# Kernel tuning notes

Measured on AMD Instinct MI355X. Metric: run time of the kernel, lower is better.

The kernel has to match this reference:

```python
import jax, jax.numpy as jnp
import numpy as np

N, E, D = 50000, 600000, 128
NEG_SLOPE = 0.2

def setup_inputs() -> dict:
    key = jax.random.key(0)
    ks = jax.random.split(key, 12)
    s = 1.0 / np.sqrt(D)
    return {
        "x": jax.random.normal(ks[0], (N, D), jnp.float32),
        "edge_index": jax.random.randint(ks[1], (2, E), 0, N),
        "edge_attr": jax.random.normal(ks[2], (E, D), jnp.float32),
        "ln1_g": jnp.ones((D,), jnp.float32),
        "ln1_b": jnp.zeros((D,), jnp.float32),
        "W_lin": jax.random.normal(ks[3], (D, D), jnp.float32) * s,
        "att_src": jax.random.normal(ks[4], (D,), jnp.float32) * s,
        "att_dst": jax.random.normal(ks[5], (D,), jnp.float32) * s,
        "W_edge": jax.random.normal(ks[6], (D, D), jnp.float32) * s,
        "att_edge": jax.random.normal(ks[7], (D,), jnp.float32) * s,
        "gat_bias": jnp.zeros((D,), jnp.float32),
        "ln2_g": jnp.ones((D,), jnp.float32),
        "ln2_b": jnp.zeros((D,), jnp.float32),
        "W1": jax.random.normal(ks[8], (D, 4 * D), jnp.float32) * s,
        "b1": jnp.zeros((4 * D,), jnp.float32),
        "W2": jax.random.normal(ks[9], (4 * D, D), jnp.float32) * (1.0 / np.sqrt(4 * D)),
        "b2": jnp.zeros((D,), jnp.float32),
    }


def _layernorm(x, g, b, eps=1e-5):
    mu = jnp.mean(x, axis=-1, keepdims=True)
    var = jnp.mean(jnp.square(x - mu), axis=-1, keepdims=True)
    return (x - mu) * jax.lax.rsqrt(var + eps) * g + b


def _gat_conv(x, edge_index, edge_attr, W_lin, att_src, att_dst, W_edge, att_edge, gat_bias):
    # PyG GATConv, heads=1, concat=False, add_self_loops=False, edge_dim=D
    src, dst = edge_index[0], edge_index[1]
    h = x @ W_lin                      # [N, D] shared src/dst projection
    a_src = h @ att_src                # [N]
    a_dst = h @ att_dst                # [N]
    a_edge = (edge_attr @ W_edge) @ att_edge  # [E]
    alpha = a_src[src] + a_dst[dst] + a_edge  # [E]
    alpha = jnp.where(alpha > 0, alpha, NEG_SLOPE * alpha)  # leaky_relu(0.2)
    # segment softmax over destination nodes
    m = jax.ops.segment_max(alpha, dst, num_segments=N)
    m = jnp.where(jnp.isfinite(m), m, 0.0)
    ex = jnp.exp(alpha - m[dst])
    denom = jax.ops.segment_sum(ex, dst, num_segments=N)
    coef = ex / jnp.maximum(denom[dst], 1e-16)
    # weighted scatter-aggregation of source messages
    out = jax.ops.segment_sum(coef[:, None] * h[src], dst, num_segments=N)
    return out + gat_bias


def reference(x, edge_index, edge_attr, ln1_g, ln1_b, W_lin, att_src, att_dst,
              W_edge, att_edge, gat_bias, ln2_g, ln2_b, W1, b1, W2, b2):
    # pre-norm + GAT message passing + residual (dropout = eval identity)
    xn = _layernorm(x, ln1_g, ln1_b)
    x = x + _gat_conv(xn, edge_index, edge_attr, W_lin, att_src, att_dst,
                      W_edge, att_edge, gat_bias)
    # pre-norm + FFN + residual
    xn = _layernorm(x, ln2_g, ln2_b)
    ffn = jax.nn.relu(xn @ W1 + b1) @ W2 + b2
    return x + ffn
```

## Files before the change

kernel.cpp:

```cpp
#include <hip/hip_runtime.h>

#define D 128
#define NEG_SLOPE 0.2f

typedef __attribute__((ext_vector_type(8))) short short8;
typedef __attribute__((ext_vector_type(4))) float f32x4;

__device__ __forceinline__ float wred_sum(float v){
#pragma unroll
  for (int m = 32; m; m >>= 1) v += __shfl_xor(v, m);
  return v;
}
__device__ __forceinline__ int wred_sumi(int v){
#pragma unroll
  for (int m = 32; m; m >>= 1) v += __shfl_xor(v, m);
  return v;
}
__device__ __forceinline__ float wred_max(float v){
#pragma unroll
  for (int m = 32; m; m >>= 1) v = fmaxf(v, __shfl_xor(v, m));
  return v;
}
__device__ __forceinline__ unsigned short bf16r(float f){
  unsigned int u = __float_as_uint(f);
  u += 0x7fffu + ((u >> 16) & 1u);
  return (unsigned short)(u >> 16);
}
__device__ __forceinline__ float bf2f(unsigned int hi16){
  return __uint_as_float(hi16 << 16);
}

__global__ void k_prep0(const float* __restrict__ W_lin, const float* __restrict__ W1,
                        const float* __restrict__ W2, const float* __restrict__ W_edge,
                        const float* __restrict__ att_edge,
                        unsigned short* __restrict__ Wlt, unsigned short* __restrict__ W1t,
                        unsigned short* __restrict__ W2t, float* __restrict__ we,
                        int* __restrict__ cnt, int N){
  int t = blockIdx.x * blockDim.x + threadIdx.x;
  if (t < N) cnt[t] = 0;
  if (t < 128 * 128){
    int c = t >> 7, k = t & 127;
    Wlt[t] = bf16r(W_lin[k * 128 + c]);
  } else if (t < 128 * 128 + 512 * 128){
    int u = t - 128 * 128; int c = u >> 7, k = u & 127;
    W1t[u] = bf16r(W1[k * 512 + c]);
  } else if (t < 128 * 128 + 512 * 128 + 128 * 512){
    int u = t - (128 * 128 + 512 * 128); int c = u >> 9, k = u & 511;
    W2t[u] = bf16r(W2[k * 128 + c]);
  } else {
    int u = t - (128 * 128 + 512 * 128 + 128 * 512);
    if (u < 128){
      float s = 0.f;
      for (int j = 0; j < 128; ++j) s += W_edge[u * 128 + j] * att_edge[j];
      we[u] = s;
    }
  }
}

__global__ __launch_bounds__(256) void k_hgemm(const float* __restrict__ x,
                                               const unsigned short* __restrict__ Wlt,
                                               const float* __restrict__ ln1_g,
                                               const float* __restrict__ ln1_b,
                                               const float* __restrict__ att_src,
                                               const float* __restrict__ att_dst,
                                               const int* __restrict__ ei,
                                               unsigned short* __restrict__ hq,
                                               float* __restrict__ asrc,
                                               float* __restrict__ adst,
                                               int* __restrict__ cnt, int N, int E){
  __shared__ unsigned short wbuf[16384];
#pragma unroll
  for (int r = 0; r < 8; ++r){
    int idx = r * 256 + threadIdx.x;
    int c = idx >> 4, kc = idx & 15;
    short8 w = *(const short8*)(Wlt + c * 128 + kc * 8);
    *(short8*)((char*)wbuf + c * 256 + ((kc * 16) ^ ((c & 7) << 4))) = w;
  }
  __syncthreads();
  int wid = threadIdx.x >> 6, lane = threadIdx.x & 63;
  int rb = blockIdx.x * 64 + wid * 16;
  int row = rb + (lane & 15);
  int rowc = row < N ? row : N - 1;
  int ksub = (lane >> 4) * 8;
  float v[4][8];
#pragma unroll
  for (int kb = 0; kb < 4; ++kb){
    float4 p0 = *(const float4*)(x + (size_t)rowc * 128 + kb * 32 + ksub);
    float4 p1 = *(const float4*)(x + (size_t)rowc * 128 + kb * 32 + ksub + 4);
    v[kb][0]=p0.x; v[kb][1]=p0.y; v[kb][2]=p0.z; v[kb][3]=p0.w;
    v[kb][4]=p1.x; v[kb][5]=p1.y; v[kb][6]=p1.z; v[kb][7]=p1.w;
  }
  float s = 0.f;
#pragma unroll
  for (int kb = 0; kb < 4; ++kb)
#pragma unroll
    for (int j = 0; j < 8; ++j) s += v[kb][j];
  s += __shfl_xor(s, 16); s += __shfl_xor(s, 32);
  float mu = s * (1.0f / 128.f);
  float q = 0.f;
#pragma unroll
  for (int kb = 0; kb < 4; ++kb)
#pragma unroll
    for (int j = 0; j < 8; ++j){ float d = v[kb][j] - mu; q += d * d; }
  q += __shfl_xor(q, 16); q += __shfl_xor(q, 32);
  float rstd = rsqrtf(q * (1.0f / 128.f) + 1e-5f);
  short8 a[4];
#pragma unroll
  for (int kb = 0; kb < 4; ++kb){
    float4 g0 = *(const float4*)(ln1_g + kb * 32 + ksub);
    float4 g1 = *(const float4*)(ln1_g + kb * 32 + ksub + 4);
    float4 b0 = *(const float4*)(ln1_b + kb * 32 + ksub);
    float4 b1 = *(const float4*)(ln1_b + kb * 32 + ksub + 4);
    float gg[8] = {g0.x,g0.y,g0.z,g0.w,g1.x,g1.y,g1.z,g1.w};
    float bb[8] = {b0.x,b0.y,b0.z,b0.w,b1.x,b1.y,b1.z,b1.w};
#pragma unroll
    for (int j = 0; j < 8; ++j)
      a[kb][j] = (short)bf16r((v[kb][j] - mu) * rstd * gg[j] + bb[j]);
  }
  f32x4 acc[8];
#pragma unroll
  for (int ct = 0; ct < 8; ++ct) acc[ct] = (f32x4){0.f, 0.f, 0.f, 0.f};
#pragma unroll
  for (int ct = 0; ct < 8; ++ct){
    int col = ct * 16 + (lane & 15);
    int cswz = (col & 7) << 4;
#pragma unroll
    for (int kb = 0; kb < 4; ++kb){
      short8 bf = *(const short8*)((const char*)wbuf + col * 256 +
                                   ((kb * 64 + ksub * 2) ^ cswz));
      acc[ct] = __builtin_amdgcn_mfma_f32_16x16x32_bf16(a[kb], bf, acc[ct], 0, 0, 0);
    }
  }
  int r0 = rb + (lane >> 4) * 4;
#pragma unroll
  for (int ct = 0; ct < 8; ++ct){
    int col = ct * 16 + (lane & 15);
#pragma unroll
    for (int j = 0; j < 4; ++j){
      int r = r0 + j;
      if (r < N) hq[(size_t)r * 128 + col] = bf16r(acc[ct][j]);
    }
  }
  float as_v[8], ad_v[8];
#pragma unroll
  for (int ct = 0; ct < 8; ++ct){
    int col = ct * 16 + (lane & 15);
    as_v[ct] = att_src[col];
    ad_v[ct] = att_dst[col];
  }
  float ps[4] = {0.f,0.f,0.f,0.f}, pd[4] = {0.f,0.f,0.f,0.f};
#pragma unroll
  for (int ct = 0; ct < 8; ++ct)
#pragma unroll
    for (int j = 0; j < 4; ++j){
      ps[j] += acc[ct][j] * as_v[ct];
      pd[j] += acc[ct][j] * ad_v[ct];
    }
#pragma unroll
  for (int m = 1; m < 16; m <<= 1)
#pragma unroll
    for (int j = 0; j < 4; ++j){
      ps[j] += __shfl_xor(ps[j], m);
      pd[j] += __shfl_xor(pd[j], m);
    }
  if ((lane & 15) == 0){
#pragma unroll
    for (int j = 0; j < 4; ++j){
      int r = r0 + j;
      if (r < N){ asrc[r] = ps[j]; adst[r] = pd[j]; }
    }
  }
  int t = blockIdx.x * blockDim.x + threadIdx.x;
  int stride = gridDim.x * blockDim.x;
  for (int e = t; e < E; e += stride) atomicAdd(&cnt[ei[E + e]], 1);
}

__global__ void k_escan(const int* __restrict__ cnt, int* __restrict__ start,
                        int* __restrict__ cursor, int N){
  int b = blockIdx.x, t = threadIdx.x;
  int base = b * 256;
  int acc = 0;
  for (int i = t; i < base; i += 256) acc += cnt[i];
  acc = wred_sumi(acc);
  __shared__ int wsum[4];
  if ((t & 63) == 0) wsum[t >> 6] = acc;
  __syncthreads();
  int s_off = wsum[0] + wsum[1] + wsum[2] + wsum[3];
  int i = base + t;
  int c = (i < N) ? cnt[i] : 0;
  __shared__ int sd[256];
  sd[t] = c;
  __syncthreads();
  for (int off = 1; off < 256; off <<= 1){
    int vv = (t >= off) ? sd[t - off] : 0;
    __syncthreads();
    sd[t] += vv;
    __syncthreads();
  }
  int st = s_off + sd[t] - c;
  if (i <= N) start[i] = st;
  if (i < N) cursor[i] = st;
}

__global__ void k_edge_scatter(const float* __restrict__ ea, const int* __restrict__ ei,
                               const float* __restrict__ we, const float* __restrict__ asrc,
                               const float* __restrict__ adst, int* __restrict__ cursor,
                               int2* __restrict__ esa, int E){
  int gw = (blockIdx.x * blockDim.x + threadIdx.x) >> 6;
  int lane = threadIdx.x & 63;
  int e = gw * 2 + (lane >> 5);
  int li = lane & 31;
  if (e >= E) return;
  float4 v = *(const float4*)(ea + (size_t)e * 128 + li * 4);
  float4 w = *(const float4*)(we + li * 4);
  float s = v.x * w.x + v.y * w.y + v.z * w.z + v.w * w.w;
#pragma unroll
  for (int m = 16; m; m >>= 1) s += __shfl_xor(s, m);
  if (li == 0){
    int sn = ei[e], dn = ei[E + e];
    float al = asrc[sn] + adst[dn] + s;
    al = al > 0.f ? al : NEG_SLOPE * al;
    int slot = atomicAdd(&cursor[dn], 1);
    esa[slot] = make_int2(sn, __float_as_int(al));
  }
}

__global__ void k_agg(const float* __restrict__ x, const unsigned short* __restrict__ hq,
                      const int* __restrict__ start, const int2* __restrict__ esa,
                      const float* __restrict__ gat_bias,
                      const float* __restrict__ g2, const float* __restrict__ b2,
                      float* __restrict__ out, unsigned short* __restrict__ xn2q, int N){
  int n = (blockIdx.x * blockDim.x + threadIdx.x) >> 6;
  int lane = threadIdx.x & 63;
  if (n >= N) return;
  int beg = start[n], end = start[n + 1];
  float m = -1e30f;
  for (int i = beg + lane; i < end; i += 64) m = fmaxf(m, __int_as_float(esa[i].y));
  m = wred_max(m);
  float ds = 0.f, a0 = 0.f, a1 = 0.f;
#pragma unroll 2
  for (int s = beg; s < end; ++s){
    int2 ev = esa[s];
    float ex = __expf(__int_as_float(ev.y) - m);
    ds += ex;
    unsigned int hv = *(const unsigned int*)(hq + (size_t)ev.x * 128 + lane * 2);
    a0 += ex * bf2f(hv & 0xffffu);
    a1 += ex * bf2f(hv >> 16);
  }
  float inv = (end > beg) ? 1.f / fmaxf(ds, 1e-16f) : 0.f;
  a0 *= inv; a1 *= inv;
  float2 xv  = *(const float2*)(x + (size_t)n * 128 + lane * 2);
  float2 gbv = *(const float2*)(gat_bias + lane * 2);
  float r0 = xv.x + a0 + gbv.x;
  float r1 = xv.y + a1 + gbv.y;
  float mu = wred_sum(r0 + r1) * (1.0f / 128.f);
  float d0 = r0 - mu, d1 = r1 - mu;
  float var = wred_sum(d0 * d0 + d1 * d1) * (1.0f / 128.f);
  float rstd = rsqrtf(var + 1e-5f);
  float2 gv = *(const float2*)(g2 + lane * 2);
  float2 bv = *(const float2*)(b2 + lane * 2);
  float o0 = d0 * rstd * gv.x + bv.x;
  float o1 = d1 * rstd * gv.y + bv.y;
  *(float2*)(out + (size_t)n * 128 + lane * 2) = make_float2(r0, r1);
  unsigned int pk = (unsigned int)bf16r(o0) | ((unsigned int)bf16r(o1) << 16);
  *(unsigned int*)(xn2q + (size_t)n * 128 + lane * 2) = pk;
}

__global__ __launch_bounds__(512) void k_ffn(const unsigned short* __restrict__ xn2q,
                                             const unsigned short* __restrict__ W1t,
                                             const unsigned short* __restrict__ W2t,
                                             const float* __restrict__ b1,
                                             const float* __restrict__ b2,
                                             float* __restrict__ out, int N, int T){
  __shared__ unsigned short w1lds[128 * 128];
  __shared__ unsigned short w2lds[128 * 128];
  __shared__ unsigned short xnt[32 * 128];
  __shared__ unsigned short hidt[32 * 128];
  const int tid = threadIdx.x;
  const int chunk = blockIdx.x & 3;
  const int tb0 = blockIdx.x >> 2;
#pragma unroll
  for (int r = 0; r < 8; ++r){
    int idx = r * 512 + tid;
    int cl = (idx >> 4) & 127, kc = idx & 15;
    int dst = cl * 256 + ((kc * 16) ^ ((cl & 7) << 4));
    if (idx < 2048){
      short8 w1v = *(const short8*)(W1t + (size_t)(chunk * 128 + cl) * 128 + kc * 8);
      *(short8*)((char*)w1lds + dst) = w1v;
    } else {
      short8 w2v = *(const short8*)(W2t + (size_t)cl * 512 + chunk * 128 + kc * 8);
      *(short8*)((char*)w2lds + dst) = w2v;
    }
  }
  const int wid = tid >> 6, lane = tid & 63;
  const int i = lane & 15, g = lane >> 4;
  const int rw = wid >> 2;
  const int ca = wid & 3;
  for (int t = tb0; t < T; t += 128){
    {
      int row = tid >> 4, kc = tid & 15;
      int trow = t * 32 + row;
      int trc = trow < N ? trow : N - 1;
      short8 xv = *(const short8*)(xn2q + (size_t)trc * 128 + kc * 8);
      *(short8*)((char*)xnt + row * 256 + ((kc * 16) ^ ((row & 7) << 4))) = xv;
    }
    __syncthreads();
#pragma unroll
    for (int ct = 0; ct < 2; ++ct){
      int hcol = ca * 32 + ct * 16 + i;
      int cswz = (hcol & 7) << 4;
      f32x4 hacc = {0.f, 0.f, 0.f, 0.f};
#pragma unroll
      for (int kb = 0; kb < 4; ++kb){
        int arow = rw * 16 + i;
        short8 af = *(const short8*)((const char*)xnt + arow * 256 +
                                     ((kb * 64 + g * 16) ^ ((arow & 7) << 4)));
        short8 bf = *(const short8*)((const char*)w1lds + hcol * 256 +
                                     ((kb * 64 + g * 16) ^ cswz));
        hacc = __builtin_amdgcn_mfma_f32_16x16x32_bf16(af, bf, hacc, 0, 0, 0);
      }
      float bias = b1[chunk * 128 + hcol];
#pragma unroll
      for (int j = 0; j < 4; ++j){
        float v = hacc[j] + bias;
        v = v > 0.f ? v : 0.f;
        int nl = rw * 16 + g * 4 + j;
        *(unsigned short*)((char*)hidt + nl * 256 + ((hcol * 2) ^ ((nl & 7) << 4))) = bf16r(v);
      }
    }
    __syncthreads();
#pragma unroll
    for (int ct = 0; ct < 2; ++ct){
      int ocol = ca * 32 + ct * 16 + i;
      int cswz = (ocol & 7) << 4;
      f32x4 oacc = {0.f, 0.f, 0.f, 0.f};
#pragma unroll
      for (int kbl = 0; kbl < 4; ++kbl){
        int nrow = rw * 16 + i;
        short8 af = *(const short8*)((const char*)hidt + nrow * 256 +
                                     ((kbl * 64 + g * 16) ^ ((nrow & 7) << 4)));
        short8 bf = *(const short8*)((const char*)w2lds + ocol * 256 +
                                     ((kbl * 64 + g * 16) ^ cswz));
        oacc = __builtin_amdgcn_mfma_f32_16x16x32_bf16(af, bf, oacc, 0, 0, 0);
      }
      float bias = (chunk == 0) ? b2[ocol] : 0.f;
#pragma unroll
      for (int j = 0; j < 4; ++j){
        int row = t * 32 + rw * 16 + g * 4 + j;
        if (row < N) atomicAdd(&out[(size_t)row * 128 + ocol], oacc[j] + bias);
      }
    }
    __syncthreads();
  }
}

extern "C" void kernel_launch(void* const* d_in, const int* in_sizes, int n_in,
                              void* d_out, int out_size, void* d_ws, size_t ws_size,
                              hipStream_t stream){
  const float* x        = (const float*)d_in[0];
  const int*   ei       = (const int*)  d_in[1];
  const float* ea       = (const float*)d_in[2];
  const float* ln1_g    = (const float*)d_in[3];
  const float* ln1_b    = (const float*)d_in[4];
  const float* W_lin    = (const float*)d_in[5];
  const float* att_src  = (const float*)d_in[6];
  const float* att_dst  = (const float*)d_in[7];
  const float* W_edge   = (const float*)d_in[8];
  const float* att_edge = (const float*)d_in[9];
  const float* gat_bias = (const float*)d_in[10];
  const float* ln2_g    = (const float*)d_in[11];
  const float* ln2_b    = (const float*)d_in[12];
  const float* W1       = (const float*)d_in[13];
  const float* b1       = (const float*)d_in[14];
  const float* W2       = (const float*)d_in[15];
  const float* b2       = (const float*)d_in[16];

  const int N = in_sizes[0] / 128;
  const int E = in_sizes[2] / 128;
  const int T32 = (N + 31) / 32;
  float* out = (float*)d_out;

  char* pp = (char*)d_ws;
  auto carve = [&](size_t bytes) -> char* {
    char* r = pp; pp += (bytes + 255) & ~(size_t)255; return r;
  };
  unsigned short* hq     = (unsigned short*)carve((size_t)N * 128 * 2);
  unsigned short* xn2q   = (unsigned short*)carve((size_t)N * 128 * 2);
  float*          asrc   = (float*)carve((size_t)N * 4);
  float*          adst   = (float*)carve((size_t)N * 4);
  int2*           esa    = (int2*)carve((size_t)E * 8);
  int*            cnt    = (int*)carve((size_t)N * 4);
  int*            cursor = (int*)carve((size_t)N * 4);
  int*            start  = (int*)carve((size_t)(N + 1) * 4);
  unsigned short* Wlt    = (unsigned short*)carve(128 * 128 * 2);
  unsigned short* W1t    = (unsigned short*)carve(512 * 128 * 2);
  unsigned short* W2t    = (unsigned short*)carve(128 * 512 * 2);
  float*          we     = (float*)carve(128 * 4);

  k_prep0<<<(128*128 + 512*128 + 128*512 + 128 + 255) / 256, 256, 0, stream>>>(
      W_lin, W1, W2, W_edge, att_edge, Wlt, W1t, W2t, we, cnt, N);
  k_hgemm<<<(N + 63) / 64, 256, 0, stream>>>(x, Wlt, ln1_g, ln1_b, att_src, att_dst, ei,
                                             hq, asrc, adst, cnt, N, E);
  k_escan<<<N / 256 + 1, 256, 0, stream>>>(cnt, start, cursor, N);
  k_edge_scatter<<<(E + 7) / 8, 256, 0, stream>>>(ea, ei, we, asrc, adst, cursor, esa, E);
  k_agg<<<(N + 3) / 4, 256, 0, stream>>>(x, hq, start, esa, gat_bias, ln2_g, ln2_b,
                                         out, xn2q, N);
  k_ffn<<<512, 512, 0, stream>>>(xn2q, W1t, W2t, b1, b2, out, N, T32);
}
```

Measured before the change: 309.2 us.

## Restructure FFN kernel into per-wave independent row tiles without tile loop syncs

The persistent FFN kernel, in which 512 blocks looped over 32-row tiles with three block barriers per tile, becomes a one-shot grid. Each 256-thread block handles 64 rows, and each wave owns 16 rows. A fragments load straight from global memory into registers, and each wave keeps a private hidden-activation buffer in LDS, so the per-tile barriers go away. In exchange, every block now reloads the 64KB of bf16 W1/W2 chunk weights into LDS for only 64 rows, which greatly raises L2-to-LDS traffic compared with the persistent version.

```diff
diff --git a/kernel.cpp b/kernel.cpp
--- a/kernel.cpp
+++ b/kernel.cpp
@@ -266,22 +266,21 @@
   *(unsigned int*)(xn2q + (size_t)n * 128 + lane * 2) = pk;
 }
 
-__global__ __launch_bounds__(512) void k_ffn(const unsigned short* __restrict__ xn2q,
+__global__ __launch_bounds__(256) void k_ffn(const unsigned short* __restrict__ xn2q,
                                              const unsigned short* __restrict__ W1t,
                                              const unsigned short* __restrict__ W2t,
                                              const float* __restrict__ b1,
                                              const float* __restrict__ b2,
-                                             float* __restrict__ out, int N, int T){
+                                             float* __restrict__ out, int N){
   __shared__ unsigned short w1lds[128 * 128];
   __shared__ unsigned short w2lds[128 * 128];
-  __shared__ unsigned short xnt[32 * 128];
-  __shared__ unsigned short hidt[32 * 128];
+  __shared__ unsigned short hidt[4 * 16 * 128];
   const int tid = threadIdx.x;
   const int chunk = blockIdx.x & 3;
-  const int tb0 = blockIdx.x >> 2;
-#pragma unroll
-  for (int r = 0; r < 8; ++r){
-    int idx = r * 512 + tid;
+  const int grp = blockIdx.x >> 2;
+#pragma unroll
+  for (int r = 0; r < 16; ++r){
+    int idx = r * 256 + tid;
     int cl = (idx >> 4) & 127, kc = idx & 15;
     int dst = cl * 256 + ((kc * 16) ^ ((cl & 7) << 4));
     if (idx < 2048){
@@ -292,65 +291,55 @@
       *(short8*)((char*)w2lds + dst) = w2v;
     }
   }
+  __syncthreads();
   const int wid = tid >> 6, lane = tid & 63;
   const int i = lane & 15, g = lane >> 4;
-  const int rw = wid >> 2;
-  const int ca = wid & 3;
-  for (int t = tb0; t < T; t += 128){
-    {
-      int row = tid >> 4, kc = tid & 15;
-      int trow = t * 32 + row;
-      int trc = trow < N ? trow : N - 1;
-      short8 xv = *(const short8*)(xn2q + (size_t)trc * 128 + kc * 8);
-      *(short8*)((char*)xnt + row * 256 + ((kc * 16) ^ ((row & 7) << 4))) = xv;
-    }
-    __syncthreads();
-#pragma unroll
-    for (int ct = 0; ct < 2; ++ct){
-      int hcol = ca * 32 + ct * 16 + i;
-      int cswz = (hcol & 7) << 4;
-      f32x4 hacc = {0.f, 0.f, 0.f, 0.f};
-#pragma unroll
-      for (int kb = 0; kb < 4; ++kb){
-        int arow = rw * 16 + i;
-        short8 af = *(const short8*)((const char*)xnt + arow * 256 +
-                                     ((kb * 64 + g * 16) ^ ((arow & 7) << 4)));
-        short8 bf = *(const short8*)((const char*)w1lds + hcol * 256 +
-                                     ((kb * 64 + g * 16) ^ cswz));
-        hacc = __builtin_amdgcn_mfma_f32_16x16x32_bf16(af, bf, hacc, 0, 0, 0);
-      }
-      float bias = b1[chunk * 128 + hcol];
-#pragma unroll
-      for (int j = 0; j < 4; ++j){
-        float v = hacc[j] + bias;
-        v = v > 0.f ? v : 0.f;
-        int nl = rw * 16 + g * 4 + j;
-        *(unsigned short*)((char*)hidt + nl * 256 + ((hcol * 2) ^ ((nl & 7) << 4))) = bf16r(v);
-      }
-    }
-    __syncthreads();
-#pragma unroll
-    for (int ct = 0; ct < 2; ++ct){
-      int ocol = ca * 32 + ct * 16 + i;
-      int cswz = (ocol & 7) << 4;
-      f32x4 oacc = {0.f, 0.f, 0.f, 0.f};
-#pragma unroll
-      for (int kbl = 0; kbl < 4; ++kbl){
-        int nrow = rw * 16 + i;
-        short8 af = *(const short8*)((const char*)hidt + nrow * 256 +
-                                     ((kbl * 64 + g * 16) ^ ((nrow & 7) << 4)));
-        short8 bf = *(const short8*)((const char*)w2lds + ocol * 256 +
-                                     ((kbl * 64 + g * 16) ^ cswz));
-        oacc = __builtin_amdgcn_mfma_f32_16x16x32_bf16(af, bf, oacc, 0, 0, 0);
-      }
-      float bias = (chunk == 0) ? b2[ocol] : 0.f;
-#pragma unroll
-      for (int j = 0; j < 4; ++j){
-        int row = t * 32 + rw * 16 + g * 4 + j;
-        if (row < N) atomicAdd(&out[(size_t)row * 128 + ocol], oacc[j] + bias);
-      }
-    }
-    __syncthreads();
+  const int row0 = grp * 64 + wid * 16;
+  char* hb = (char*)hidt + wid * 4096;
+  int arow = row0 + i;
+  int arc = arow < N ? arow : N - 1;
+  short8 a[4];
+#pragma unroll
+  for (int kb = 0; kb < 4; ++kb)
+    a[kb] = *(const short8*)(xn2q + (size_t)arc * 128 + kb * 32 + g * 8);
+#pragma unroll
+  for (int ct = 0; ct < 8; ++ct){
+    int hcol = ct * 16 + i;
+    int cswz = (hcol & 7) << 4;
+    f32x4 hacc = {0.f, 0.f, 0.f, 0.f};
+#pragma unroll
+    for (int kb = 0; kb < 4; ++kb){
+      short8 bf = *(const short8*)((const char*)w1lds + hcol * 256 +
+                                   ((kb * 64 + g * 16) ^ cswz));
+      hacc = __builtin_amdgcn_mfma_f32_16x16x32_bf16(a[kb], bf, hacc, 0, 0, 0);
+    }
+    float bias = b1[chunk * 128 + hcol];
+#pragma unroll
+    for (int j = 0; j < 4; ++j){
+      float v = hacc[j] + bias;
+      v = v > 0.f ? v : 0.f;
+      int nl = g * 4 + j;
+      *(unsigned short*)(hb + nl * 256 + ((hcol * 2) ^ ((nl & 7) << 4))) = bf16r(v);
+    }
+  }
+#pragma unroll
+  for (int ct = 0; ct < 8; ++ct){
+    int ocol = ct * 16 + i;
+    int cswz = (ocol & 7) << 4;
+    f32x4 oacc = {0.f, 0.f, 0.f, 0.f};
+#pragma unroll
+    for (int kbl = 0; kbl < 4; ++kbl){
+      short8 af = *(const short8*)(hb + i * 256 + ((kbl * 64 + g * 16) ^ ((i & 7) << 4)));
+      short8 bf = *(const short8*)((const char*)w2lds + ocol * 256 +
+                                   ((kbl * 64 + g * 16) ^ cswz));
+      oacc = __builtin_amdgcn_mfma_f32_16x16x32_bf16(af, bf, oacc, 0, 0, 0);
+    }
+    float bias = (chunk == 0) ? b2[ocol] : 0.f;
+#pragma unroll
+    for (int j = 0; j < 4; ++j){
+      int row = row0 + g * 4 + j;
+      if (row < N) atomicAdd(&out[(size_t)row * 128 + ocol], oacc[j] + bias);
+    }
   }
 }
 
@@ -377,7 +366,7 @@
 
   const int N = in_sizes[0] / 128;
   const int E = in_sizes[2] / 128;
-  const int T32 = (N + 31) / 32;
+  const int G64 = (N + 63) / 64;
   float* out = (float*)d_out;
 
   char* pp = (char*)d_ws;
@@ -405,5 +394,5 @@
   k_edge_scatter<<<(E + 7) / 8, 256, 0, stream>>>(ea, ei, we, asrc, adst, cursor, esa, E);
   k_agg<<<(N + 3) / 4, 256, 0, stream>>>(x, hq, start, esa, gat_bias, ln2_g, ln2_b,
                                          out, xn2q, N);
-  k_ffn<<<512, 512, 0, stream>>>(xn2q, W1t, W2t, b1, b2, out, N, T32);
-}
+  k_ffn<<<4 * G64, 256, 0, stream>>>(xn2q, W1t, W2t, b1, b2, out, N);
+}
```

Result: slower. 346.6 us (+12.1%).

## Unroll GAT aggregation gathers by eight and software-pipeline FFN tile loads

Applied to the files above, without the earlier changes.

The aggregation kernel now issues eight edge-record loads and eight neighbour-feature gathers at a time and keeps eight independent partial accumulators, so more memory requests are in flight per wave. The FFN kernel prefetches the next tile's normalized activations into registers while the current tile's second GEMM runs, and drops one barrier per iteration. The cost is higher register pressure in both kernels and a changed floating-point summation order in the softmax aggregation.

```diff
diff --git a/kernel.cpp b/kernel.cpp
--- a/kernel.cpp
+++ b/kernel.cpp
@@ -237,16 +237,39 @@
   float m = -1e30f;
   for (int i = beg + lane; i < end; i += 64) m = fmaxf(m, __int_as_float(esa[i].y));
   m = wred_max(m);
-  float ds = 0.f, a0 = 0.f, a1 = 0.f;
-#pragma unroll 2
-  for (int s = beg; s < end; ++s){
+  float dsv[8] = {0,0,0,0,0,0,0,0};
+  float a0v[8] = {0,0,0,0,0,0,0,0};
+  float a1v[8] = {0,0,0,0,0,0,0,0};
+  int s = beg;
+  for (; s + 8 <= end; s += 8){
+    int2 ev[8];
+#pragma unroll
+    for (int u = 0; u < 8; ++u) ev[u] = esa[s + u];
+    float xv[8];
+    unsigned int hv[8];
+#pragma unroll
+    for (int u = 0; u < 8; ++u){
+      xv[u] = __expf(__int_as_float(ev[u].y) - m);
+      hv[u] = *(const unsigned int*)(hq + (size_t)ev[u].x * 128 + lane * 2);
+    }
+#pragma unroll
+    for (int u = 0; u < 8; ++u){
+      dsv[u] += xv[u];
+      a0v[u] += xv[u] * bf2f(hv[u] & 0xffffu);
+      a1v[u] += xv[u] * bf2f(hv[u] >> 16);
+    }
+  }
+  for (; s < end; ++s){
     int2 ev = esa[s];
     float ex = __expf(__int_as_float(ev.y) - m);
-    ds += ex;
     unsigned int hv = *(const unsigned int*)(hq + (size_t)ev.x * 128 + lane * 2);
-    a0 += ex * bf2f(hv & 0xffffu);
-    a1 += ex * bf2f(hv >> 16);
-  }
+    dsv[0] += ex;
+    a0v[0] += ex * bf2f(hv & 0xffffu);
+    a1v[0] += ex * bf2f(hv >> 16);
+  }
+  float ds = ((dsv[0]+dsv[1])+(dsv[2]+dsv[3])) + ((dsv[4]+dsv[5])+(dsv[6]+dsv[7]));
+  float a0 = ((a0v[0]+a0v[1])+(a0v[2]+a0v[3])) + ((a0v[4]+a0v[5])+(a0v[6]+a0v[7]));
+  float a1 = ((a1v[0]+a1v[1])+(a1v[2]+a1v[3])) + ((a1v[4]+a1v[5])+(a1v[6]+a1v[7]));
   float inv = (end > beg) ? 1.f / fmaxf(ds, 1e-16f) : 0.f;
   a0 *= inv; a1 *= inv;
   float2 xv  = *(const float2*)(x + (size_t)n * 128 + lane * 2);
@@ -296,15 +319,9 @@
   const int i = lane & 15, g = lane >> 4;
   const int rw = wid >> 2;
   const int ca = wid & 3;
-  for (int t = tb0; t < T; t += 128){
-    {
-      int row = tid >> 4, kc = tid & 15;
-      int trow = t * 32 + row;
-      int trc = trow < N ? trow : N - 1;
-      short8 xv = *(const short8*)(xn2q + (size_t)trc * 128 + kc * 8);
-      *(short8*)((char*)xnt + row * 256 + ((kc * 16) ^ ((row & 7) << 4))) = xv;
-    }
-    __syncthreads();
+  const int srow = tid >> 4, skc = tid & 15;
+
+  auto phaseA = [&](){
 #pragma unroll
     for (int ct = 0; ct < 2; ++ct){
       int hcol = ca * 32 + ct * 16 + i;
@@ -328,7 +345,8 @@
         *(unsigned short*)((char*)hidt + nl * 256 + ((hcol * 2) ^ ((nl & 7) << 4))) = bf16r(v);
       }
     }
-    __syncthreads();
+  };
+  auto phaseB = [&](int t){
 #pragma unroll
     for (int ct = 0; ct < 2; ++ct){
       int ocol = ca * 32 + ct * 16 + i;
@@ -350,8 +368,34 @@
         if (row < N) atomicAdd(&out[(size_t)row * 128 + ocol], oacc[j] + bias);
       }
     }
+  };
+  auto stage_load = [&](int t)->short8 {
+    int trow = t * 32 + srow;
+    int trc = trow < N ? trow : N - 1;
+    return *(const short8*)(xn2q + (size_t)trc * 128 + skc * 8);
+  };
+  auto stage_write = [&](short8 xv){
+    *(short8*)((char*)xnt + srow * 256 + ((skc * 16) ^ ((srow & 7) << 4))) = xv;
+  };
+
+  int t = tb0;
+  {
+    short8 xv = stage_load(t);
+    stage_write(xv);
+  }
+  __syncthreads();
+  phaseA();
+  __syncthreads();
+  for (int tn = t + 128; tn < T; tn += 128){
+    short8 xv = stage_load(tn);
+    phaseB(t);
+    stage_write(xv);
     __syncthreads();
-  }
+    phaseA();
+    __syncthreads();
+    t = tn;
+  }
+  phaseB(t);
 }
 
 extern "C" void kernel_launch(void* const* d_in, const int* in_sizes, int n_in,
```

Result: no change. 308.8 us (-0.1%).
